# Kernel tuning notes

Hardware: AMD Instinct MI355X
Metric: run time of the kernel (lower is better)

The kernel has to match this reference:

```python
import jax, jax.numpy as jnp
import numpy as np

B, V, D, NH, DH = 1, 6, 256, 8, 32
L, ZP = 4, 4
BEV = 80
Q = BEV * BEV
SHAPES = [(56, 100), (28, 50), (14, 25), (7, 13)]
N = sum(h * w for h, w in SHAPES)
PAD_H, PAD_W = 448, 800
PC = (-48.0, -48.0, -5.0, 48.0, 48.0, 3.0)
EPS = 1e-5


def _ref3d():
    # get_reference_points + pc_range scaling; the original overwrites the z channel
    # with scaled-x (code bug: ref_3d[...,2:3] = ref_3d[...,:1]*zrange+zmin) -> reproduced faithfully,
    # so all ZP pillar points are identical.
    u = jnp.arange(Q)
    xs = ((u % BEV).astype(jnp.float32) + 0.5) / BEV
    ys = ((u // BEV).astype(jnp.float32) + 0.5) / BEV
    x = xs * (PC[3] - PC[0]) + PC[0]
    y = ys * (PC[4] - PC[1]) + PC[1]
    z = x * (PC[5] - PC[2]) + PC[2]
    p = jnp.stack([x, y, z], -1)  # [Q,3]
    return jnp.broadcast_to(p[None], (ZP, Q, 3))


def _project(l2i):
    # l2i: [B,V,4,4] -> normalized coords [B,V,Q,ZP,2], validity mask [B,V,Q,ZP]
    pts = _ref3d().reshape(-1, 3)
    pts_h = jnp.concatenate([pts, jnp.ones_like(pts[:, :1])], -1)  # [ZP*Q,4]
    ip = jnp.einsum('bvij,nj->bvni', l2i, pts_h)                   # [B,V,ZP*Q,4]
    zc = ip[..., 2]
    xy = ip[..., :2] / jnp.clip(zc, EPS, None)[..., None]
    xn = xy[..., 0] / PAD_W
    yn = xy[..., 1] / PAD_H
    m = (zc > EPS) & (xn > 0) & (xn < 1) & (yn > 0) & (yn < 1)
    coords = jnp.stack([xn, yn], -1).reshape(B, V, ZP, Q, 2).transpose(0, 1, 3, 2, 4)
    mask = m.reshape(B, V, ZP, Q).transpose(0, 1, 3, 2)
    return coords, mask


def _forward(feat0, feat1, feat2, feat3, lidar2img_mat, bev_emb, level_embeds,
             view_embeds, value_W, value_b, off_W, off_b, aw_W, aw_b, out_W, out_b):
    feats = [feat0, feat1, feat2, feat3]
    parts = []
    for l, f in enumerate(feats):
        h, w = SHAPES[l]
        x = f.reshape(B, V, D, h * w).transpose(0, 1, 3, 2)  # [B,V,hw,D]
        x = x + view_embeds[None, :, None, :] + level_embeds[l]
        parts.append(x)
    feat_flat = jnp.concatenate(parts, axis=2)  # [B,V,N,D]

    coords, mask = _project(lidar2img_mat)
    mask_any = mask.any(-1)                                            # [B,V,Q]
    count = jnp.clip(mask_any.sum(1).astype(jnp.float32), 1.0, None)   # [B,Q]

    value = (feat_flat.reshape(B * V, N, D) @ value_W + value_b).reshape(B * V, N, NH, DH)
    off = (bev_emb @ off_W + off_b).reshape(Q, NH, L, ZP, 2)
    aw = jax.nn.softmax((bev_emb @ aw_W + aw_b).reshape(Q, NH, L * ZP), -1).reshape(Q, NH, L, ZP)
    ref = coords.reshape(B * V, Q, ZP, 2)

    out = jnp.zeros((B * V, Q, NH, DH), feat_flat.dtype)
    start = 0
    for l, (h, w) in enumerate(SHAPES):
        v_l = value[:, start:start + h * w].transpose(0, 2, 1, 3).reshape(B * V * NH, h * w, DH)
        start += h * w
        loc = ref[:, :, None, :, :] + off[None, :, :, l] / jnp.array([w, h], feat_flat.dtype)
        loc = loc.transpose(0, 2, 1, 3, 4).reshape(B * V * NH, Q * ZP, 2)
        # grid_sample(align_corners=False, padding='zeros') with grid 2*loc-1
        gx = loc[..., 0] * w - 0.5
        gy = loc[..., 1] * h - 0.5
        x0 = jnp.floor(gx).astype(jnp.int32)
        y0 = jnp.floor(gy).astype(jnp.int32)
        wx1 = gx - x0
        wy1 = gy - y0

        def corner(xi, yi, wt):
            valid = (xi >= 0) & (xi < w) & (yi >= 0) & (yi < h)
            lin = jnp.clip(yi, 0, h - 1) * w + jnp.clip(xi, 0, w - 1)
            g = jnp.take_along_axis(v_l, lin[..., None], axis=1)
            return g * (wt * valid)[..., None]

        s = (corner(x0, y0, (1 - wx1) * (1 - wy1)) + corner(x0 + 1, y0, wx1 * (1 - wy1))
             + corner(x0, y0 + 1, (1 - wx1) * wy1) + corner(x0 + 1, y0 + 1, wx1 * wy1))
        s = s.reshape(B * V, NH, Q, ZP, DH)
        out = out + jnp.einsum('vhqzd,qhz->vqhd', s, aw[:, :, l])

    attn = out.reshape(B, V, Q, D)
    slots = (attn * mask_any[..., None]).sum(1) / count[..., None]
    slots = slots @ out_W + out_b
    return bev_emb[None] + slots  # dropout is identity at inference


def setup_inputs() -> dict:
    key = jax.random.key(0)
    ks = jax.random.split(key, 16)
    s = 0.02
    return {
        'feat0': jax.random.normal(ks[0], (B, V, D) + SHAPES[0], jnp.float32),
        'feat1': jax.random.normal(ks[1], (B, V, D) + SHAPES[1], jnp.float32),
        'feat2': jax.random.normal(ks[2], (B, V, D) + SHAPES[2], jnp.float32),
        'feat3': jax.random.normal(ks[3], (B, V, D) + SHAPES[3], jnp.float32),
        'lidar2img_mat': jax.random.normal(ks[4], (B, V, 4, 4), jnp.float32) * 50.0,
        'bev_emb': jax.random.normal(ks[5], (Q, D), jnp.float32) * s,
        'level_embeds': jax.random.normal(ks[6], (L, D), jnp.float32) * s,
        'view_embeds': jax.random.normal(ks[7], (V, D), jnp.float32) * s,
        'value_W': jax.random.normal(ks[8], (D, D), jnp.float32) * s,
        'value_b': jnp.zeros((D,), jnp.float32),
        'off_W': jax.random.normal(ks[9], (D, NH * L * ZP * 2), jnp.float32) * s,
        'off_b': jnp.zeros((NH * L * ZP * 2,), jnp.float32),
        'aw_W': jax.random.normal(ks[10], (D, NH * L * ZP), jnp.float32) * s,
        'aw_b': jnp.zeros((NH * L * ZP,), jnp.float32),
        'out_W': jax.random.normal(ks[11], (D, D), jnp.float32) * s,
        'out_b': jnp.zeros((D,), jnp.float32),
    }


def reference(feat0, feat1, feat2, feat3, lidar2img_mat, bev_emb, level_embeds,
              view_embeds, value_W, value_b, off_W, off_b, aw_W, aw_b, out_W, out_b):
    return _forward(feat0, feat1, feat2, feat3, lidar2img_mat, bev_emb, level_embeds,
                    view_embeds, value_W, value_b, off_W, off_b, aw_W, aw_b, out_W, out_b)
```

## Files before the change

### kernel.cpp

```cpp
#include <hip/hip_runtime.h>
#include <cstdint>
#include <cstddef>

#define NV 6
#define ND 256
#define NHEAD 8
#define NBEV 80
#define NQ 6400
#define NTOK 7441
#define MROWS (NV * NTOK)
#define MROWSP 44672
#define FEPS 1e-5f

#define VBLKS 698
#define GBLKS 848
#define GCHUNK (GBLKS / 8)

#define PR_PROJ 150
#define PR_TR   2832
#define PR_BEV  800
#define PB0 PR_PROJ
#define PB1 (PB0 + PR_TR)
#define PB2 (PB1 + PR_BEV)
#define PB3 (PB2 + 256)
#define PB4 (PB3 + 256)
#define PB5 (PB4 + 128)
#define PB6 (PB5 + 256)
#define PBT (PB6 + 24)

typedef __attribute__((ext_vector_type(8))) short bfx8;
typedef __attribute__((ext_vector_type(4))) float fx4;

typedef __attribute__((address_space(3))) unsigned int lds_u32_t;
typedef __attribute__((address_space(1))) const unsigned int glb_u32_t;

__device__ __forceinline__ void gload16(const unsigned short* g, unsigned short* l) {
    __builtin_amdgcn_global_load_lds((glb_u32_t*)g, (lds_u32_t*)l, 16, 0, 0);
}

__device__ __forceinline__ unsigned short f2bf(float x) {
    uint32_t u = __builtin_bit_cast(uint32_t, x);
    u += 0x7FFFu + ((u >> 16) & 1u);
    return (unsigned short)(u >> 16);
}
__device__ __forceinline__ float lof(uint32_t u) {
    return __builtin_bit_cast(float, u << 16);
}
__device__ __forceinline__ float hif(uint32_t u) {
    return __builtin_bit_cast(float, u & 0xFFFF0000u);
}
__device__ __forceinline__ unsigned short f2h(float x) {
    return __builtin_bit_cast(unsigned short, (_Float16)x);
}
__device__ __forceinline__ float h2f(unsigned short h) {
    return (float)__builtin_bit_cast(_Float16, h);
}

__global__ __launch_bounds__(256) void k_prep(
        const float* __restrict__ f0, const float* __restrict__ f1,
        const float* __restrict__ f2, const float* __restrict__ f3,
        const float* __restrict__ l2i, const float* __restrict__ bev,
        const float* __restrict__ ve, const float* __restrict__ le,
        const float* __restrict__ vW, const float* __restrict__ vB,
        const float* __restrict__ oW, const float* __restrict__ aW,
        const float* __restrict__ outW,
        float2* __restrict__ coords, int* __restrict__ mask,
        unsigned short* __restrict__ featT, unsigned short* __restrict__ bevh,
        unsigned short* __restrict__ vWt, unsigned short* __restrict__ oaWt,
        unsigned short* __restrict__ outWt, float* __restrict__ emb_proj) {
    int bid = blockIdx.x;
    int t = threadIdx.x;
    if (bid < PB0) {
        int idx = bid * 256 + t;
        int v = idx / NQ, q = idx - v * NQ;
        float xs = ((float)(q % NBEV) + 0.5f) / (float)NBEV;
        float ys = ((float)(q / NBEV) + 0.5f) / (float)NBEV;
        float x = xs * 96.0f - 48.0f;
        float y = ys * 96.0f - 48.0f;
        float z = x * 8.0f - 5.0f;
        const float* M = l2i + v * 16;
        float ip0 = M[0] * x + M[1] * y + M[2] * z + M[3];
        float ip1 = M[4] * x + M[5] * y + M[6] * z + M[7];
        float ip2 = M[8] * x + M[9] * y + M[10] * z + M[11];
        float dz = fmaxf(ip2, FEPS);
        float xn = ip0 / dz / 800.0f;
        float yn = ip1 / dz / 448.0f;
        bool m = (ip2 > FEPS) && (xn > 0.0f) && (xn < 1.0f) && (yn > 0.0f) && (yn < 1.0f);
        coords[idx] = make_float2(xn, yn);
        mask[idx] = m ? 1 : 0;
    } else if (bid < PB1) {
        __shared__ float T[64][65];
        int idx = bid - PB0;
        int v = idx / 472;
        int rem = idx - v * 472;
        int mt = rem >> 2, kt = rem & 3;
        int hw, p0, st;
        const float* base;
        if (mt < 88)       { base = f0; hw = 5600; st = 0;    p0 = mt * 64; }
        else if (mt < 110) { base = f1; hw = 1400; st = 5600; p0 = (mt - 88) * 64; }
        else if (mt < 116) { base = f2; hw = 350;  st = 7000; p0 = (mt - 110) * 64; }
        else               { base = f3; hw = 91;   st = 7350; p0 = (mt - 116) * 64; }
        int k0 = kt * 64;
        const float* src = base + (size_t)v * 256 * hw;
#pragma unroll
        for (int i = 0; i < 16; ++i) {
            int ii = t + i * 256;
            int kk = ii >> 6, mm = ii & 63;
            float val = (p0 + mm < hw) ? src[(size_t)(k0 + kk) * hw + p0 + mm] : 0.0f;
            T[kk][mm] = val;
        }
        __syncthreads();
        size_t row0 = (size_t)v * NTOK + st + p0;
        int slot = t & 7;
#pragma unroll
        for (int j = 0; j < 2; ++j) {
            int mm = (t >> 3) + j * 32;
            if (p0 + mm < hw) {
                bfx8 o;
#pragma unroll
                for (int jj = 0; jj < 8; ++jj)
                    o[jj] = (short)f2bf(T[slot * 8 + jj][mm]);
                *(bfx8*)&featT[(row0 + mm) * 256 + k0 + slot * 8] = o;
            }
        }
    } else if (bid < PB2) {
        size_t e = (size_t)(bid - PB1) * 2048 + t * 8;
        float4 a = *(const float4*)(bev + e);
        float4 b = *(const float4*)(bev + e + 4);
        bfx8 o;
        o[0] = (short)f2bf(a.x); o[1] = (short)f2bf(a.y);
        o[2] = (short)f2bf(a.z); o[3] = (short)f2bf(a.w);
        o[4] = (short)f2bf(b.x); o[5] = (short)f2bf(b.y);
        o[6] = (short)f2bf(b.z); o[7] = (short)f2bf(b.w);
        *(bfx8*)(bevh + e) = o;
    } else if (bid < PB3) {
        int e = (bid - PB2) * 256 + t;
        int k = e >> 8, n = e & 255;
        vWt[(size_t)n * 256 + k] = f2bf(vW[(size_t)k * 256 + n]);
    } else if (bid < PB4) {
        int e = (bid - PB3) * 256 + t;
        int k = e >> 8, n = e & 255;
        oaWt[(size_t)n * 256 + k] = f2bf(oW[(size_t)k * 256 + n]);
    } else if (bid < PB5) {
        int e = (bid - PB4) * 256 + t;
        int k = e >> 7, n = e & 127;
        oaWt[(size_t)(256 + n) * 256 + k] = f2bf(aW[(size_t)k * 128 + n]);
    } else if (bid < PB6) {
        int e = (bid - PB5) * 256 + t;
        int k = e >> 8, n = e & 255;
        outWt[(size_t)n * 256 + k] = f2bf(outW[(size_t)k * 256 + n]);
    } else {
        int blk = bid - PB6;
        int v = blk >> 2, l = blk & 3;
        float acc = vB[t];
        for (int d = 0; d < ND; ++d)
            acc += (ve[v * ND + d] + le[l * ND + d]) * vW[d * ND + t];
        emb_proj[blk * ND + t] = acc;
    }
}

__global__ __launch_bounds__(256) void k_gemms(
        const unsigned short* __restrict__ featT,
        const unsigned short* __restrict__ vWt, const float* __restrict__ emb_proj,
        unsigned short* __restrict__ value,
        const unsigned short* __restrict__ bevh,
        const unsigned short* __restrict__ oaWt,
        const float* __restrict__ oB, const float* __restrict__ aB,
        float* __restrict__ off, float* __restrict__ aw_pre) {
    __shared__ unsigned short LDS[4 * 8192];
    int b = blockIdx.x;
    int lb = (b & 7) * GCHUNK + (b >> 3);
    int t = threadIdx.x;
    int lane = t & 63, w = t >> 6;
    int wm = w >> 1, wn = w & 1;
    int lr = lane & 15, lk = lane >> 4;

    bool isval = lb < VBLKS;
    int m0, c0;
    const unsigned short *ap, *bp;
    if (isval) {
        m0 = (lb >> 1) * 128; c0 = (lb & 1) * 128;
        ap = featT; bp = vWt;
    } else {
        int r6 = lb - VBLKS;
        m0 = (r6 / 3) * 128; c0 = (r6 % 3) * 128;
        ap = bevh; bp = oaWt;
    }

    int rsub = lane >> 3;
    int kslx = (lane & 7) ^ rsub;
    const unsigned short* asrc = ap + (size_t)(m0 + w * 32 + rsub) * 256 + kslx * 8;
    const unsigned short* bsrc = bp + (size_t)(c0 + w * 32 + rsub) * 256 + kslx * 8;

    fx4 acc[4][4];
#pragma unroll
    for (int i = 0; i < 4; ++i)
#pragma unroll
        for (int j = 0; j < 4; ++j) acc[i][j] = (fx4)0.0f;

    auto STAGE = [&](int c, int buf) {
        const unsigned short* a = asrc + c * 64;
        const unsigned short* bb = bsrc + c * 64;
        unsigned short* la = &LDS[(buf * 2 + 0) * 8192 + w * 2048];
        unsigned short* lbp = &LDS[(buf * 2 + 1) * 8192 + w * 2048];
#pragma unroll
        for (int j = 0; j < 4; ++j) {
            gload16(a + j * 2048, la + j * 512);
            gload16(bb + j * 2048, lbp + j * 512);
        }
    };
    auto COMPUTE = [&](int buf) {
        const char* Ab = (const char*)&LDS[(buf * 2 + 0) * 8192] + (wm * 64 + lr) * 128;
        const char* Bb = (const char*)&LDS[(buf * 2 + 1) * 8192] + (wn * 64 + lr) * 128;
#pragma unroll
        for (int s = 0; s < 2; ++s) {
            int xs = (((s * 4 + lk) ^ (lr & 7)) << 4);
            bfx8 bfv[4];
#pragma unroll
            for (int f = 0; f < 4; ++f)
                bfv[f] = *(const bfx8*)(Bb + f * 2048 + xs);
#pragma unroll
            for (int fm = 0; fm < 4; ++fm) {
                bfx8 afv = *(const bfx8*)(Ab + fm * 2048 + xs);
#pragma unroll
                for (int fn = 0; fn < 4; ++fn)
                    acc[fm][fn] = __builtin_amdgcn_mfma_f32_16x16x32_bf16(
                        afv, bfv[fn], acc[fm][fn], 0, 0, 0);
            }
        }
    };

    STAGE(0, 0);
#pragma unroll
    for (int c = 0; c < 4; ++c) {
        __syncthreads();
        if (c < 3) STAGE(c + 1, (c + 1) & 1);
        COMPUTE(c & 1);
    }

    if (isval) {
#pragma unroll
        for (int fm = 0; fm < 4; ++fm) {
#pragma unroll
            for (int r = 0; r < 4; ++r) {
                int m = m0 + wm * 64 + fm * 16 + lk * 4 + r;
                if (m >= MROWS) continue;
                int v = m / NTOK;
                int n = m - v * NTOK;
                int l = (n < 5600) ? 0 : (n < 7000) ? 1 : (n < 7350) ? 2 : 3;
                const float* ep = emb_proj + (size_t)(v * 4 + l) * ND;
#pragma unroll
                for (int fn = 0; fn < 4; ++fn) {
                    int col = c0 + wn * 64 + fn * 16 + lr;
                    value[(size_t)m * ND + col] = f2bf(acc[fm][fn][r] + ep[col]);
                }
            }
        }
    } else if (c0 < 256) {
#pragma unroll
        for (int fm = 0; fm < 4; ++fm) {
#pragma unroll
            for (int fn = 0; fn < 4; ++fn) {
                int col = c0 + wn * 64 + fn * 16 + lr;
                float bs = oB[col];
#pragma unroll
                for (int r = 0; r < 4; ++r) {
                    int m = m0 + wm * 64 + fm * 16 + lk * 4 + r;
                    off[(size_t)m * 256 + col] = acc[fm][fn][r] + bs;
                }
            }
        }
    } else {
#pragma unroll
        for (int fm = 0; fm < 4; ++fm) {
#pragma unroll
            for (int fn = 0; fn < 4; ++fn) {
                int col = wn * 64 + fn * 16 + lr;
                float bs = aB[col];
#pragma unroll
                for (int r = 0; r < 4; ++r) {
                    int m = m0 + wm * 64 + fm * 16 + lk * 4 + r;
                    aw_pre[(size_t)m * 128 + col] = acc[fm][fn][r] + bs;
                }
            }
        }
    }
}

#define SQB 2
__global__ __launch_bounds__(256) void k_sample(
        const float2* __restrict__ coords, const int* __restrict__ mask,
        const float* __restrict__ off, const float* __restrict__ awlog,
        const unsigned short* __restrict__ value, float* __restrict__ slots) {
    __shared__ float aw_s[SQB][128];
    __shared__ uint4 lw_s[SQB][NV][128];
    __shared__ float2 cxy_s[SQB][NV];
    __shared__ int msk_s[SQB][NV];

    int b = blockIdx.x;
    int lb = (b & 7) * (NQ / SQB / 8) + (b >> 3);
    int q0 = lb * SQB;
    int t = threadIdx.x;
    if (t < SQB * NV) {
        int qq = t / NV, v = t - qq * NV;
        msk_s[qq][v] = mask[v * NQ + q0 + qq];
        cxy_s[qq][v] = coords[v * NQ + q0 + qq];
    }
    {
        int qq = t >> 7, c2 = t & 127;
        aw_s[qq][c2] = awlog[(size_t)(q0 + qq) * 128 + c2];
    }
    __syncthreads();
    if (t < SQB * NHEAD) {
        int qq = t >> 3, h = t & 7;
        float* p = &aw_s[qq][h * 16];
        float mx = p[0];
#pragma unroll
        for (int i = 1; i < 16; ++i) mx = fmaxf(mx, p[i]);
        float e[16];
        float s = 0.0f;
#pragma unroll
        for (int i = 0; i < 16; ++i) { e[i] = __expf(p[i] - mx); s += e[i]; }
        float inv = 1.0f / s;
#pragma unroll
        for (int i = 0; i < 16; ++i) p[i] = e[i] * inv;
    }
    __syncthreads();

    const int LW[4] = {100, 50, 25, 13};
    const int LH[4] = {56, 28, 14, 7};
    const int LST[4] = {0, 5600, 7000, 7350};
    for (int idx = t; idx < SQB * NV * 128; idx += 256) {
        int c2 = idx & 127;
        int rem = idx >> 7;
        int qq = rem / NV, v = rem - qq * NV;
        if (!msk_s[qq][v]) continue;
        int ll = (c2 >> 2) & 3;
        int iwl = LW[ll], ihl = LH[ll], st = LST[ll];
        float wl = (float)iwl, hl = (float)ihl;
        float2 o2 = *(const float2*)&off[(size_t)(q0 + qq) * 256 + 2 * c2];
        float2 cc = cxy_s[qq][v];
        float gx = cc.x * wl + o2.x - 0.5f;
        float gy = cc.y * hl + o2.y - 0.5f;
        float fxf = floorf(gx), fyf = floorf(gy);
        int x0 = (int)fxf, y0 = (int)fyf;
        float wx = gx - fxf, wy = gy - fyf;
        bool bx0 = (unsigned)x0 < (unsigned)iwl;
        bool bx1 = (unsigned)(x0 + 1) < (unsigned)iwl;
        bool by0 = (unsigned)y0 < (unsigned)ihl;
        bool by1 = (unsigned)(y0 + 1) < (unsigned)ihl;
        int cx0 = min(max(x0, 0), iwl - 1);
        int cx1 = min(max(x0 + 1, 0), iwl - 1);
        int cy0 = min(max(y0, 0), ihl - 1);
        int cy1 = min(max(y0 + 1, 0), ihl - 1);
        float wa = aw_s[qq][c2];
        int r0 = st + cy0 * iwl, r1 = st + cy1 * iwl;
        float w00 = (bx0 && by0) ? (1.0f - wx) * (1.0f - wy) * wa : 0.0f;
        float w01 = (bx1 && by0) ? wx * (1.0f - wy) * wa : 0.0f;
        float w10 = (bx0 && by1) ? (1.0f - wx) * wy * wa : 0.0f;
        float w11 = (bx1 && by1) ? wx * wy * wa : 0.0f;
        uint4 lw;
        lw.x = (uint32_t)(unsigned short)(r0 + cx0) | ((uint32_t)(unsigned short)(r0 + cx1) << 16);
        lw.y = (uint32_t)(unsigned short)(r1 + cx0) | ((uint32_t)(unsigned short)(r1 + cx1) << 16);
        lw.z = (uint32_t)f2h(w00) | ((uint32_t)f2h(w01) << 16);
        lw.w = (uint32_t)f2h(w10) | ((uint32_t)f2h(w11) << 16);
        lw_s[qq][v][c2] = lw;
    }
    __syncthreads();

    int qq = t >> 7, cp = t & 127;
    int hb = (cp >> 4) * 16;
    float acc0 = 0.0f, acc1 = 0.0f;
    int cnt = 0;
#pragma unroll
    for (int v = 0; v < NV; ++v) cnt += msk_s[qq][v];
    for (int v = 0; v < NV; ++v) {
        if (!msk_s[qq][v]) continue;
        const uint32_t* vb = (const uint32_t*)(value + (size_t)v * NTOK * 256) + cp;
#pragma unroll
        for (int ci = 0; ci < 16; ++ci) {
            uint4 lw = lw_s[qq][v][hb + ci];
            uint32_t u0 = vb[(size_t)(lw.x & 0xFFFF) * 128];
            uint32_t u1 = vb[(size_t)(lw.x >> 16) * 128];
            uint32_t u2 = vb[(size_t)(lw.y & 0xFFFF) * 128];
            uint32_t u3 = vb[(size_t)(lw.y >> 16) * 128];
            float w0 = h2f((unsigned short)(lw.z & 0xFFFF));
            float w1 = h2f((unsigned short)(lw.z >> 16));
            float w2 = h2f((unsigned short)(lw.w & 0xFFFF));
            float w3 = h2f((unsigned short)(lw.w >> 16));
            acc0 += w0 * lof(u0) + w1 * lof(u1) + w2 * lof(u2) + w3 * lof(u3);
            acc1 += w0 * hif(u0) + w1 * hif(u1) + w2 * hif(u2) + w3 * hif(u3);
        }
    }
    float invc = 1.0f / fmaxf((float)cnt, 1.0f);
    *(float2*)&slots[(size_t)(q0 + qq) * 256 + 2 * cp] = make_float2(acc0 * invc, acc1 * invc);
}

__global__ __launch_bounds__(256) void k_out(
        const float* __restrict__ A, const unsigned short* __restrict__ Bt,
        const float* __restrict__ bias, const float* __restrict__ addsrc,
        float* __restrict__ out) {
    __shared__ unsigned short As[64][40];
    __shared__ unsigned short Bs[128][40];
    int t = threadIdx.x;
    int m0 = blockIdx.x * 64, c0 = blockIdx.y * 128;
    int lane = t & 63, w = t >> 6;
    int wm = w >> 1, wn = w & 1;
    int lr = lane & 15, lk = lane >> 4;
    int mA = t & 63, kg = t >> 6;
    const float* ap = A + (size_t)(m0 + mA) * 256 + kg * 8;
    const unsigned short* bp = Bt + (size_t)(c0 + (t >> 1)) * 256 + (t & 1) * 16;
    fx4 acc[2][4];
#pragma unroll
    for (int i = 0; i < 2; ++i)
#pragma unroll
        for (int j = 0; j < 4; ++j) acc[i][j] = (fx4)0.0f;

    float4 va0 = *(const float4*)ap;
    float4 va1 = *(const float4*)(ap + 4);
    bfx8 brg = *(const bfx8*)bp;
    bfx8 brg2 = *(const bfx8*)(bp + 8);
#pragma unroll
    for (int k0 = 0; k0 < 256; k0 += 32) {
        bfx8 a8;
        a8[0] = (short)f2bf(va0.x); a8[1] = (short)f2bf(va0.y);
        a8[2] = (short)f2bf(va0.z); a8[3] = (short)f2bf(va0.w);
        a8[4] = (short)f2bf(va1.x); a8[5] = (short)f2bf(va1.y);
        a8[6] = (short)f2bf(va1.z); a8[7] = (short)f2bf(va1.w);
        *(bfx8*)&As[mA][kg * 8] = a8;
        *(bfx8*)&Bs[t >> 1][(t & 1) * 16] = brg;
        *(bfx8*)&Bs[t >> 1][(t & 1) * 16 + 8] = brg2;
        __syncthreads();
        if (k0 < 224) {
            va0 = *(const float4*)(ap + k0 + 32);
            va1 = *(const float4*)(ap + k0 + 36);
            brg = *(const bfx8*)(bp + k0 + 32);
            brg2 = *(const bfx8*)(bp + k0 + 40);
        }
        bfx8 bfv[4];
#pragma unroll
        for (int f = 0; f < 4; ++f)
            bfv[f] = *(bfx8*)&Bs[wn * 64 + f * 16 + lr][lk * 8];
#pragma unroll
        for (int fm = 0; fm < 2; ++fm) {
            bfx8 afv = *(bfx8*)&As[wm * 32 + fm * 16 + lr][lk * 8];
#pragma unroll
            for (int fn = 0; fn < 4; ++fn)
                acc[fm][fn] = __builtin_amdgcn_mfma_f32_16x16x32_bf16(
                    afv, bfv[fn], acc[fm][fn], 0, 0, 0);
        }
        __syncthreads();
    }
#pragma unroll
    for (int fm = 0; fm < 2; ++fm) {
#pragma unroll
        for (int fn = 0; fn < 4; ++fn) {
            int col = c0 + wn * 64 + fn * 16 + lr;
            float bs = bias[col];
#pragma unroll
            for (int r = 0; r < 4; ++r) {
                int m = m0 + wm * 32 + fm * 16 + lk * 4 + r;
                out[(size_t)m * 256 + col] =
                    acc[fm][fn][r] + bs + addsrc[(size_t)m * 256 + col];
            }
        }
    }
}

extern "C" void kernel_launch(void* const* d_in, const int* in_sizes, int n_in,
                              void* d_out, int out_size, void* d_ws, size_t ws_size,
                              hipStream_t stream) {
    const float* f0   = (const float*)d_in[0];
    const float* f1   = (const float*)d_in[1];
    const float* f2   = (const float*)d_in[2];
    const float* f3   = (const float*)d_in[3];
    const float* l2i  = (const float*)d_in[4];
    const float* bev  = (const float*)d_in[5];
    const float* le   = (const float*)d_in[6];
    const float* ve   = (const float*)d_in[7];
    const float* vW   = (const float*)d_in[8];
    const float* vB   = (const float*)d_in[9];
    const float* oW   = (const float*)d_in[10];
    const float* oB   = (const float*)d_in[11];
    const float* aW   = (const float*)d_in[12];
    const float* aB   = (const float*)d_in[13];
    const float* outW = (const float*)d_in[14];
    const float* outB = (const float*)d_in[15];
    float* out = (float*)d_out;

    char* ws = (char*)d_ws;
    size_t o = 0;
    auto alloc = [&](size_t bytes) {
        void* p = ws + o;
        o += (bytes + 255) & ~(size_t)255;
        return p;
    };
    float2* coords   = (float2*)alloc((size_t)NV * NQ * sizeof(float2));
    int*    mask     = (int*)alloc((size_t)NV * NQ * sizeof(int));
    float*  emb_proj = (float*)alloc((size_t)24 * ND * sizeof(float));
    float*  off      = (float*)alloc((size_t)NQ * 256 * sizeof(float));
    float*  aw_pre   = (float*)alloc((size_t)NQ * 128 * sizeof(float));
    float*  slots    = (float*)alloc((size_t)NQ * 256 * sizeof(float));
    unsigned short* value = (unsigned short*)alloc((size_t)MROWS * ND * sizeof(short));
    unsigned short* featT = (unsigned short*)alloc((size_t)MROWSP * ND * sizeof(short));
    unsigned short* bevh  = (unsigned short*)alloc((size_t)NQ * ND * sizeof(short));
    unsigned short* vWt   = (unsigned short*)alloc((size_t)256 * 256 * sizeof(short));
    unsigned short* oaWt  = (unsigned short*)alloc((size_t)384 * 256 * sizeof(short));
    unsigned short* outWt = (unsigned short*)alloc((size_t)256 * 256 * sizeof(short));

    k_prep<<<PBT, 256, 0, stream>>>(f0, f1, f2, f3, l2i, bev, ve, le, vW, vB,
                                    oW, aW, outW, coords, mask, featT, bevh,
                                    vWt, oaWt, outWt, emb_proj);
    k_gemms<<<GBLKS, 256, 0, stream>>>(featT, vWt, emb_proj, value,
                                       bevh, oaWt, oB, aB, off, aw_pre);
    k_sample<<<NQ / SQB, 256, 0, stream>>>(coords, mask, off, aw_pre, value, slots);
    dim3 gout(NQ / 64, 2);
    k_out<<<gout, 256, 0, stream>>>(slots, outWt, outB, bev, out);
}
```

Before: 181.2 us.

## Fuse output projection into sampling kernel and drop separate GEMM launch

Folds the final output linear layer into the sampling kernel. Each block keeps its two queries' slot vectors in shared memory and computes the 256 outputs with scalar FMAs over bf16 weights, adding the bias and residual inline. This removes the slots buffer round trip through global memory and one kernel launch. In exchange each block re-reads the full 128KB output weight matrix per pair of queries, relying on cache, and gives up MFMA for plain FMA. It also unrolls the small embedding-projection loop in the prep kernel.

```diff
diff --git a/kernel.cpp b/kernel.cpp
--- a/kernel.cpp
+++ b/kernel.cpp
@@ -153,6 +153,7 @@
         int blk = bid - PB6;
         int v = blk >> 2, l = blk & 3;
         float acc = vB[t];
+#pragma unroll 8
         for (int d = 0; d < ND; ++d)
             acc += (ve[v * ND + d] + le[l * ND + d]) * vW[d * ND + t];
         emb_proj[blk * ND + t] = acc;
@@ -291,9 +292,13 @@
 __global__ __launch_bounds__(256) void k_sample(
         const float2* __restrict__ coords, const int* __restrict__ mask,
         const float* __restrict__ off, const float* __restrict__ awlog,
-        const unsigned short* __restrict__ value, float* __restrict__ slots) {
+        const unsigned short* __restrict__ value,
+        const unsigned short* __restrict__ outWt,
+        const float* __restrict__ outB, const float* __restrict__ bev,
+        float* __restrict__ out) {
     __shared__ float aw_s[SQB][128];
     __shared__ uint4 lw_s[SQB][NV][128];
+    __shared__ float slots_s[SQB][256];
     __shared__ float2 cxy_s[SQB][NV];
     __shared__ int msk_s[SQB][NV];
 
@@ -368,102 +373,60 @@
     }
     __syncthreads();
 
-    int qq = t >> 7, cp = t & 127;
-    int hb = (cp >> 4) * 16;
-    float acc0 = 0.0f, acc1 = 0.0f;
-    int cnt = 0;
-#pragma unroll
-    for (int v = 0; v < NV; ++v) cnt += msk_s[qq][v];
-    for (int v = 0; v < NV; ++v) {
-        if (!msk_s[qq][v]) continue;
-        const uint32_t* vb = (const uint32_t*)(value + (size_t)v * NTOK * 256) + cp;
-#pragma unroll
-        for (int ci = 0; ci < 16; ++ci) {
-            uint4 lw = lw_s[qq][v][hb + ci];
-            uint32_t u0 = vb[(size_t)(lw.x & 0xFFFF) * 128];
-            uint32_t u1 = vb[(size_t)(lw.x >> 16) * 128];
-            uint32_t u2 = vb[(size_t)(lw.y & 0xFFFF) * 128];
-            uint32_t u3 = vb[(size_t)(lw.y >> 16) * 128];
-            float w0 = h2f((unsigned short)(lw.z & 0xFFFF));
-            float w1 = h2f((unsigned short)(lw.z >> 16));
-            float w2 = h2f((unsigned short)(lw.w & 0xFFFF));
-            float w3 = h2f((unsigned short)(lw.w >> 16));
-            acc0 += w0 * lof(u0) + w1 * lof(u1) + w2 * lof(u2) + w3 * lof(u3);
-            acc1 += w0 * hif(u0) + w1 * hif(u1) + w2 * hif(u2) + w3 * hif(u3);
-        }
-    }
-    float invc = 1.0f / fmaxf((float)cnt, 1.0f);
-    *(float2*)&slots[(size_t)(q0 + qq) * 256 + 2 * cp] = make_float2(acc0 * invc, acc1 * invc);
-}
-
-__global__ __launch_bounds__(256) void k_out(
-        const float* __restrict__ A, const unsigned short* __restrict__ Bt,
-        const float* __restrict__ bias, const float* __restrict__ addsrc,
-        float* __restrict__ out) {
-    __shared__ unsigned short As[64][40];
-    __shared__ unsigned short Bs[128][40];
-    int t = threadIdx.x;
-    int m0 = blockIdx.x * 64, c0 = blockIdx.y * 128;
-    int lane = t & 63, w = t >> 6;
-    int wm = w >> 1, wn = w & 1;
-    int lr = lane & 15, lk = lane >> 4;
-    int mA = t & 63, kg = t >> 6;
-    const float* ap = A + (size_t)(m0 + mA) * 256 + kg * 8;
-    const unsigned short* bp = Bt + (size_t)(c0 + (t >> 1)) * 256 + (t & 1) * 16;
-    fx4 acc[2][4];
-#pragma unroll
-    for (int i = 0; i < 2; ++i)
-#pragma unroll
-        for (int j = 0; j < 4; ++j) acc[i][j] = (fx4)0.0f;
-
-    float4 va0 = *(const float4*)ap;
-    float4 va1 = *(const float4*)(ap + 4);
-    bfx8 brg = *(const bfx8*)bp;
-    bfx8 brg2 = *(const bfx8*)(bp + 8);
-#pragma unroll
-    for (int k0 = 0; k0 < 256; k0 += 32) {
-        bfx8 a8;
-        a8[0] = (short)f2bf(va0.x); a8[1] = (short)f2bf(va0.y);
-        a8[2] = (short)f2bf(va0.z); a8[3] = (short)f2bf(va0.w);
-        a8[4] = (short)f2bf(va1.x); a8[5] = (short)f2bf(va1.y);
-        a8[6] = (short)f2bf(va1.z); a8[7] = (short)f2bf(va1.w);
-        *(bfx8*)&As[mA][kg * 8] = a8;
-        *(bfx8*)&Bs[t >> 1][(t & 1) * 16] = brg;
-        *(bfx8*)&Bs[t >> 1][(t & 1) * 16 + 8] = brg2;
-        __syncthreads();
-        if (k0 < 224) {
-            va0 = *(const float4*)(ap + k0 + 32);
-            va1 = *(const float4*)(ap + k0 + 36);
-            brg = *(const bfx8*)(bp + k0 + 32);
-            brg2 = *(const bfx8*)(bp + k0 + 40);
-        }
-        bfx8 bfv[4];
-#pragma unroll
-        for (int f = 0; f < 4; ++f)
-            bfv[f] = *(bfx8*)&Bs[wn * 64 + f * 16 + lr][lk * 8];
-#pragma unroll
-        for (int fm = 0; fm < 2; ++fm) {
-            bfx8 afv = *(bfx8*)&As[wm * 32 + fm * 16 + lr][lk * 8];
-#pragma unroll
-            for (int fn = 0; fn < 4; ++fn)
-                acc[fm][fn] = __builtin_amdgcn_mfma_f32_16x16x32_bf16(
-                    afv, bfv[fn], acc[fm][fn], 0, 0, 0);
-        }
-        __syncthreads();
-    }
-#pragma unroll
-    for (int fm = 0; fm < 2; ++fm) {
-#pragma unroll
-        for (int fn = 0; fn < 4; ++fn) {
-            int col = c0 + wn * 64 + fn * 16 + lr;
-            float bs = bias[col];
-#pragma unroll
-            for (int r = 0; r < 4; ++r) {
-                int m = m0 + wm * 32 + fm * 16 + lk * 4 + r;
-                out[(size_t)m * 256 + col] =
-                    acc[fm][fn][r] + bs + addsrc[(size_t)m * 256 + col];
-            }
-        }
+    {
+        int qq = t >> 7, cp = t & 127;
+        int hb = (cp >> 4) * 16;
+        float acc0 = 0.0f, acc1 = 0.0f;
+        int cnt = 0;
+#pragma unroll
+        for (int v = 0; v < NV; ++v) cnt += msk_s[qq][v];
+        for (int v = 0; v < NV; ++v) {
+            if (!msk_s[qq][v]) continue;
+            const uint32_t* vb = (const uint32_t*)(value + (size_t)v * NTOK * 256) + cp;
+#pragma unroll
+            for (int ci = 0; ci < 16; ++ci) {
+                uint4 lw = lw_s[qq][v][hb + ci];
+                uint32_t u0 = vb[(size_t)(lw.x & 0xFFFF) * 128];
+                uint32_t u1 = vb[(size_t)(lw.x >> 16) * 128];
+                uint32_t u2 = vb[(size_t)(lw.y & 0xFFFF) * 128];
+                uint32_t u3 = vb[(size_t)(lw.y >> 16) * 128];
+                float w0 = h2f((unsigned short)(lw.z & 0xFFFF));
+                float w1 = h2f((unsigned short)(lw.z >> 16));
+                float w2 = h2f((unsigned short)(lw.w & 0xFFFF));
+                float w3 = h2f((unsigned short)(lw.w >> 16));
+                acc0 += w0 * lof(u0) + w1 * lof(u1) + w2 * lof(u2) + w3 * lof(u3);
+                acc1 += w0 * hif(u0) + w1 * hif(u1) + w2 * hif(u2) + w3 * hif(u3);
+            }
+        }
+        float invc = 1.0f / fmaxf((float)cnt, 1.0f);
+        slots_s[qq][2 * cp] = acc0 * invc;
+        slots_s[qq][2 * cp + 1] = acc1 * invc;
+    }
+    __syncthreads();
+
+    {
+        const unsigned short* wrow = outWt + (size_t)t * 256;
+        float ob = outB[t];
+        float y0 = ob + bev[(size_t)q0 * 256 + t];
+        float y1 = ob + bev[(size_t)(q0 + 1) * 256 + t];
+#pragma unroll 4
+        for (int d = 0; d < 256; d += 8) {
+            uint4 wu = __builtin_bit_cast(uint4, *(const bfx8*)(wrow + d));
+            float4 s0a = *(const float4*)&slots_s[0][d];
+            float4 s0b = *(const float4*)&slots_s[0][d + 4];
+            float4 s1a = *(const float4*)&slots_s[1][d];
+            float4 s1b = *(const float4*)&slots_s[1][d + 4];
+            float w0 = lof(wu.x), w1 = hif(wu.x);
+            float w2 = lof(wu.y), w3 = hif(wu.y);
+            float w4 = lof(wu.z), w5 = hif(wu.z);
+            float w6 = lof(wu.w), w7 = hif(wu.w);
+            y0 += s0a.x * w0 + s0a.y * w1 + s0a.z * w2 + s0a.w * w3
+                + s0b.x * w4 + s0b.y * w5 + s0b.z * w6 + s0b.w * w7;
+            y1 += s1a.x * w0 + s1a.y * w1 + s1a.z * w2 + s1a.w * w3
+                + s1b.x * w4 + s1b.y * w5 + s1b.z * w6 + s1b.w * w7;
+        }
+        out[(size_t)q0 * 256 + t] = y0;
+        out[(size_t)(q0 + 1) * 256 + t] = y1;
     }
 }
 
@@ -500,7 +463,6 @@
     float*  emb_proj = (float*)alloc((size_t)24 * ND * sizeof(float));
     float*  off      = (float*)alloc((size_t)NQ * 256 * sizeof(float));
     float*  aw_pre   = (float*)alloc((size_t)NQ * 128 * sizeof(float));
-    float*  slots    = (float*)alloc((size_t)NQ * 256 * sizeof(float));
     unsigned short* value = (unsigned short*)alloc((size_t)MROWS * ND * sizeof(short));
     unsigned short* featT = (unsigned short*)alloc((size_t)MROWSP * ND * sizeof(short));
     unsigned short* bevh  = (unsigned short*)alloc((size_t)NQ * ND * sizeof(short));
@@ -513,7 +475,6 @@
                                     vWt, oaWt, outWt, emb_proj);
     k_gemms<<<GBLKS, 256, 0, stream>>>(featT, vWt, emb_proj, value,
                                        bevh, oaWt, oB, aB, off, aw_pre);
-    k_sample<<<NQ / SQB, 256, 0, stream>>>(coords, mask, off, aw_pre, value, slots);
-    dim3 gout(NQ / 64, 2);
-    k_out<<<gout, 256, 0, stream>>>(slots, outWt, outB, bev, out);
-}
+    k_sample<<<NQ / SQB, 256, 0, stream>>>(coords, mask, off, aw_pre, value,
+                                           outWt, outB, bev, out);
+}
```

After: 211.1 us. +16.5%, slower.
